# Kernel optimization log

Hardware: AMD Instinct MI355X
Metric: run time of the kernel (lower is better)

Reference implementation:

```python
import jax, jax.numpy as jnp
import numpy as np

N_HEADS = 8
NEG_INF = -1e9


def setup_inputs() -> dict:
    key = jax.random.key(0)
    ks = jax.random.split(key, 9)
    B, S, D = 4, 2048, 512
    scale = 1.0 / np.sqrt(D)
    x = jax.random.normal(ks[0], (B, S, D), dtype=jnp.float32)
    mask = jnp.tril(jnp.ones((S, S), dtype=bool))[None, None, :, :]  # causal [1,1,S,S]
    W_Q_w = jax.random.normal(ks[1], (D, D), dtype=jnp.float32) * scale
    W_Q_b = jax.random.normal(ks[2], (D,), dtype=jnp.float32) * 0.02
    W_K_w = jax.random.normal(ks[3], (D, D), dtype=jnp.float32) * scale
    W_K_b = jax.random.normal(ks[4], (D,), dtype=jnp.float32) * 0.02
    W_V_w = jax.random.normal(ks[5], (D, D), dtype=jnp.float32) * scale
    W_V_b = jax.random.normal(ks[6], (D,), dtype=jnp.float32) * 0.02
    W_O_w = jax.random.normal(ks[7], (D, D), dtype=jnp.float32) * scale
    W_O_b = jax.random.normal(ks[8], (D,), dtype=jnp.float32) * 0.02
    return {"x": x, "mask": mask,
            "W_Q_w": W_Q_w, "W_Q_b": W_Q_b, "W_K_w": W_K_w, "W_K_b": W_K_b,
            "W_V_w": W_V_w, "W_V_b": W_V_b, "W_O_w": W_O_w, "W_O_b": W_O_b}


def reference(x, mask, W_Q_w, W_Q_b, W_K_w, W_K_b, W_V_w, W_V_b, W_O_w, W_O_b):
    B, S, D = x.shape
    H = N_HEADS
    Dh = D // H
    # projections (torch Linear: x @ W.T + b), split heads -> [B,H,S,Dh]
    def split_heads(t):
        return t.reshape(B, S, H, Dh).transpose(0, 2, 1, 3)
    Q = split_heads(x @ W_Q_w.T + W_Q_b)
    K = split_heads(x @ W_K_w.T + W_K_b)
    V = split_heads(x @ W_V_w.T + W_V_b)
    # scaled dot-product attention with explicit [B,H,S,S] scores
    scores = jnp.einsum("bhqd,bhkd->bhqk", Q, K) / jnp.sqrt(jnp.float32(Dh))
    scores = jnp.where(mask, scores, jnp.float32(NEG_INF))
    att = jax.nn.softmax(scores, axis=-1)
    out = jnp.einsum("bhqk,bhkd->bhqd", att, V)
    out = out.transpose(0, 2, 1, 3).reshape(B, S, D)
    return out @ W_O_w.T + W_O_b
```

## Files before the change

kernel.cpp:

```cpp
#include <hip/hip_runtime.h>
#include <hip/hip_bf16.h>

#define BATCH 4
#define SEQ   2048
#define DIM   512
#define NH    8
#define DH    64
#define NTOK  (BATCH*SEQ)

typedef __bf16 bf16x8 __attribute__((ext_vector_type(8)));
typedef float  f32x4  __attribute__((ext_vector_type(4)));

#define MFMA16(a,b,c) __builtin_amdgcn_mfma_f32_16x16x32_bf16((a),(b),(c),0,0,0)

#if __has_builtin(__builtin_amdgcn_exp2f)
#define EXP2F(x) __builtin_amdgcn_exp2f(x)
#else
#define EXP2F(x) exp2f(x)
#endif

#define QSCALE 0.18033688011112042f
#define SMAX 16.0f

typedef __attribute__((address_space(1))) void GAS;
typedef __attribute__((address_space(3))) void LAS;
__device__ __forceinline__ void gl_lds16(const void* g, void* l) {
  __builtin_amdgcn_global_load_lds((GAS*)g, (LAS*)l, 16, 0, 0);
}

__global__ __launch_bounds__(256) void cvt_all(
    const float* __restrict__ x,
    const float* __restrict__ s0, const float* __restrict__ s1,
    const float* __restrict__ s2, const float* __restrict__ s3,
    __bf16* __restrict__ xb,
    __bf16* __restrict__ o0, __bf16* __restrict__ o1,
    __bf16* __restrict__ o2, __bf16* __restrict__ o3) {
  const int i = blockIdx.x * 256 + threadIdx.x;
  const float* src;
  __bf16* dst;
  int off;
  if (i < 524288) {
    src = x; dst = xb; off = i;
  } else {
    const int j = i - 524288;
    const int which = j >> 15; off = j & 32767;
    src = (which == 0) ? s0 : (which == 1) ? s1 : (which == 2) ? s2 : s3;
    dst = (which == 0) ? o0 : (which == 1) ? o1 : (which == 2) ? o2 : o3;
  }
  const float4* s = (const float4*)src;
  float4 a = s[2*off], b = s[2*off+1];
  bf16x8 o;
  o[0] = (__bf16)a.x; o[1] = (__bf16)a.y; o[2] = (__bf16)a.z; o[3] = (__bf16)a.w;
  o[4] = (__bf16)b.x; o[5] = (__bf16)b.y; o[6] = (__bf16)b.z; o[7] = (__bf16)b.w;
  *(bf16x8*)&dst[8*off] = o;
}

__global__ __launch_bounds__(256) void gemm_qkv(
    const __bf16* __restrict__ xb,
    const __bf16* __restrict__ wq, const __bf16* __restrict__ wk,
    const __bf16* __restrict__ wv,
    const float* __restrict__ bq, const float* __restrict__ bk,
    const float* __restrict__ bv,
    __bf16* __restrict__ Qb, __bf16* __restrict__ Kb, __bf16* __restrict__ Vt)
{
  const int z = blockIdx.z;
  const __bf16* W    = (z == 0) ? wq : (z == 1) ? wk : wv;
  const float*  bias = (z == 0) ? bq : (z == 1) ? bk : bv;

  __shared__ __align__(16) __bf16 smem[128*152];
  __bf16* As = smem;
  __bf16* Bs = smem + 128*64;

  const int tid  = threadIdx.x;
  const int m0   = blockIdx.x * 128, n0 = blockIdx.y * 128;
  const int w    = tid >> 6, lane = tid & 63, quad = lane >> 4, l16 = lane & 15;
  const int wm   = (w >> 1) * 64, wn = (w & 1) * 64;
  const int srow = w*32 + (lane >> 3);
  const int scc  = (lane & 7) * 8;

  f32x4 acc[4][4] = {};

  for (int k0 = 0; k0 < DIM; k0 += 64) {
#pragma unroll
    for (int i = 0; i < 4; ++i) {
      const int row = srow + i*8;
      gl_lds16(&xb[(size_t)(m0+row)*DIM + k0 + scc], &As[(w*4+i)*512]);
      gl_lds16(&W [(size_t)(n0+row)*DIM + k0 + scc], &Bs[(w*4+i)*512]);
    }
    __syncthreads();
#pragma unroll
    for (int kk = 0; kk < 2; ++kk) {
      const int ko = kk*32 + quad*8;
      bf16x8 af[4], bfr[4];
#pragma unroll
      for (int f = 0; f < 4; ++f) {
        af[f]  = *(const bf16x8*)&As[(wm + f*16 + l16)*64 + ko];
        bfr[f] = *(const bf16x8*)&Bs[(wn + f*16 + l16)*64 + ko];
      }
#pragma unroll
      for (int fm = 0; fm < 4; ++fm)
#pragma unroll
        for (int fn = 0; fn < 4; ++fn)
          acc[fm][fn] = MFMA16(af[fm], bfr[fn], acc[fm][fn]);
    }
    __syncthreads();
  }

  __bf16* Cs = smem;
#pragma unroll
  for (int fm = 0; fm < 4; ++fm) {
#pragma unroll
    for (int fn = 0; fn < 4; ++fn) {
      const int cl  = wn + fn*16 + l16;
      const float bc = bias[n0 + cl];
#pragma unroll
      for (int r = 0; r < 4; ++r) {
        const int rl = wm + fm*16 + quad*4 + r;
        float v = acc[fm][fn][r] + bc;
        if (z == 0) v *= QSCALE;
        Cs[rl*152 + cl] = (__bf16)v;
      }
    }
  }
  __syncthreads();

  if (z < 2) {
    const int r  = tid >> 1, hh = tid & 1;
    const int grow = m0 + r, b = grow >> 11, s = grow & 2047;
    const int h  = (n0 >> 6) + hh;
    __bf16* O = (z == 0) ? Qb : Kb;
    __bf16* dst = O + ((size_t)(b*NH + h)*SEQ + s)*DH;
    const __bf16* srcr = &Cs[r*152 + hh*64];
#pragma unroll
    for (int j = 0; j < 8; ++j)
      *(bf16x8*)&dst[j*8] = *(const bf16x8*)&srcr[j*8];
  } else {
    const int c  = tid >> 1, hh = tid & 1;
    const int col = n0 + c, h = col >> 6, dh = col & 63;
    const int b  = m0 >> 11, sbase = (m0 & 2047) + hh*64;
    __bf16* dst = Vt + ((size_t)(b*NH + h)*DH + dh)*SEQ + sbase;
#pragma unroll
    for (int j8 = 0; j8 < 8; ++j8) {
      bf16x8 o;
#pragma unroll
      for (int e = 0; e < 8; ++e)
        o[e] = Cs[(hh*64 + j8*8 + e)*152 + c];
      *(bf16x8*)&dst[j8*8] = o;
    }
  }
}

__global__ __launch_bounds__(256) void gemm_out(
    const __bf16* __restrict__ attnb, const __bf16* __restrict__ wo,
    const float* __restrict__ bo, float* __restrict__ out)
{
  __shared__ __align__(16) __bf16 As[64*64];
  __shared__ __align__(16) __bf16 Bs[128*64];

  const int tid = threadIdx.x;
  const int m0  = blockIdx.x * 64, n0 = blockIdx.y * 128;
  const int w   = tid >> 6, lane = tid & 63, quad = lane >> 4, l16 = lane & 15;
  const int wm  = (w >> 1) * 32, wn = (w & 1) * 64;
  const int srow = w*8 + (lane >> 3);
  const int scc  = (lane & 7) * 8;

  f32x4 acc[2][4] = {};

  for (int k0 = 0; k0 < DIM; k0 += 64) {
#pragma unroll
    for (int i = 0; i < 2; ++i)
      gl_lds16(&attnb[(size_t)(m0 + srow + i*32)*DIM + k0 + scc],
               &As[(i*4 + w)*512]);
#pragma unroll
    for (int i = 0; i < 4; ++i)
      gl_lds16(&wo[(size_t)(n0 + srow + i*32)*DIM + k0 + scc],
               &Bs[(i*4 + w)*512]);
    __syncthreads();
#pragma unroll
    for (int kk = 0; kk < 2; ++kk) {
      const int ko = kk*32 + quad*8;
      bf16x8 af[2], bfr[4];
#pragma unroll
      for (int f = 0; f < 2; ++f)
        af[f]  = *(const bf16x8*)&As[(wm + f*16 + l16)*64 + ko];
#pragma unroll
      for (int f = 0; f < 4; ++f)
        bfr[f] = *(const bf16x8*)&Bs[(wn + f*16 + l16)*64 + ko];
#pragma unroll
      for (int fm = 0; fm < 2; ++fm)
#pragma unroll
        for (int fn = 0; fn < 4; ++fn)
          acc[fm][fn] = MFMA16(af[fm], bfr[fn], acc[fm][fn]);
    }
    __syncthreads();
  }

#pragma unroll
  for (int fm = 0; fm < 2; ++fm) {
#pragma unroll
    for (int fn = 0; fn < 4; ++fn) {
      const int col  = n0 + wn + fn*16 + l16;
      const float bc = bo[col];
#pragma unroll
      for (int r = 0; r < 4; ++r) {
        const int row = m0 + wm + fm*16 + quad*4 + r;
        out[(size_t)row*DIM + col] = acc[fm][fn][r] + bc;
      }
    }
  }
}

__global__ __launch_bounds__(64) void flash_attn(
    const __bf16* __restrict__ Qb, const __bf16* __restrict__ Kb,
    const __bf16* __restrict__ Vt, __bf16* __restrict__ attnb)
{
  const int idx = blockIdx.x;
  const int bh  = idx & 31;
  const int t   = 63 - (idx >> 5);
  const int b   = bh >> 3, h = bh & 7;
  const int lane = threadIdx.x & 63, quad = lane >> 4, l16 = lane & 15;
  const int q0  = t * 32;

  const __bf16* Qp = Qb + (size_t)bh * SEQ * DH;
  const __bf16* Kp = Kb + (size_t)bh * SEQ * DH;
  const __bf16* Vp = Vt + (size_t)bh * DH * SEQ;

  __shared__ __align__(16) __bf16 Pw[32*88];

  bf16x8 qf[2][2];
#pragma unroll
  for (int mf = 0; mf < 2; ++mf)
#pragma unroll
    for (int kk = 0; kk < 2; ++kk)
      qf[mf][kk] = *(const bf16x8*)&Qp[(size_t)(q0 + mf*16 + l16)*DH + kk*32 + quad*8];

  f32x4 of[2][4] = {};
  float l_[2][4];
#pragma unroll
  for (int mf = 0; mf < 2; ++mf)
#pragma unroll
    for (int r = 0; r < 4; ++r) l_[mf][r] = 0.f;

  const int ktiles = (q0 >> 6) + 1;

  bf16x8 kfA[4][2], kfB[4][2];
#pragma unroll
  for (int fn = 0; fn < 4; ++fn)
#pragma unroll
    for (int kk = 0; kk < 2; ++kk)
      kfA[fn][kk] = *(const bf16x8*)&Kp[(size_t)(fn*16 + l16)*DH + kk*32 + quad*8];

#define TILE_STEP(KC, KN, KT)                                                  \
  {                                                                            \
    const int k0 = (KT) * 64;                                                  \
                   \
    bf16x8 vf[4][2];                                                           \
    _Pragma("unroll")                                                          \
    for (int nd = 0; nd < 4; ++nd)                                             \
      _Pragma("unroll")                                                        \
      for (int kq = 0; kq < 2; ++kq)                                           \
        vf[nd][kq] = *(const bf16x8*)&Vp[(size_t)(nd*16 + l16)*SEQ + k0 +      \
                                         kq*32 + quad*8];                      \
                               \
    {                                                                          \
      const int kn0 = ((KT) + 1 < ktiles) ? k0 + 64 : 0;                       \
      _Pragma("unroll")                                                        \
      for (int fn = 0; fn < 4; ++fn)                                           \
        _Pragma("unroll")                                                      \
        for (int kk = 0; kk < 2; ++kk)                                         \
          KN[fn][kk] = *(const bf16x8*)&Kp[(size_t)(kn0 + fn*16 + l16)*DH +    \
                                           kk*32 + quad*8];                    \
    }                                                                          \
                                   \
    f32x4 sf[2][4] = {};                                                       \
    __builtin_amdgcn_s_setprio(1);                                             \
    _Pragma("unroll")                                                          \
    for (int mf = 0; mf < 2; ++mf)                                             \
      _Pragma("unroll")                                                        \
      for (int fn = 0; fn < 4; ++fn) {                                         \
        sf[mf][fn] = MFMA16(qf[mf][0], KC[fn][0], sf[mf][fn]);                 \
        sf[mf][fn] = MFMA16(qf[mf][1], KC[fn][1], sf[mf][fn]);                 \
      }                                                                        \
    __builtin_amdgcn_s_setprio(0);                                             \
                               \
    if (k0 + 63 > q0) {                                                        \
      _Pragma("unroll")                                                        \
      for (int mf = 0; mf < 2; ++mf)                                           \
        _Pragma("unroll")                                                      \
        for (int fn = 0; fn < 4; ++fn) {                                       \
          const int col = k0 + fn*16 + l16;                                    \
          _Pragma("unroll")                                                    \
          for (int r = 0; r < 4; ++r) {                                        \
            const int row = q0 + mf*16 + quad*4 + r;                           \
            if (col > row) sf[mf][fn][r] = -1e30f;                             \
          }                                                                    \
        }                                                                      \
    }                                                                          \
                         \
    _Pragma("unroll")                                                          \
    for (int mf = 0; mf < 2; ++mf)                                             \
      _Pragma("unroll")                                                        \
      for (int fn = 0; fn < 4; ++fn)                                           \
        _Pragma("unroll")                                                      \
        for (int r = 0; r < 4; ++r)                                            \
          sf[mf][fn][r] = EXP2F(sf[mf][fn][r] - SMAX);                         \
    _Pragma("unroll")                                                          \
    for (int mf = 0; mf < 2; ++mf)                                             \
      _Pragma("unroll")                                                        \
      for (int r = 0; r < 4; ++r)                                              \
        l_[mf][r] += (sf[mf][0][r] + sf[mf][1][r]) +                           \
                     (sf[mf][2][r] + sf[mf][3][r]);                            \
                                           \
    _Pragma("unroll")                                                          \
    for (int mf = 0; mf < 2; ++mf)                                             \
      _Pragma("unroll")                                                        \
      for (int fn = 0; fn < 4; ++fn)                                           \
        _Pragma("unroll")                                                      \
        for (int r = 0; r < 4; ++r)                                            \
          Pw[(mf*16 + quad*4 + r)*88 + fn*16 + l16] = (__bf16)sf[mf][fn][r];   \
    bf16x8 pa[2][2];                                                           \
    _Pragma("unroll")                                                          \
    for (int mf = 0; mf < 2; ++mf)                                             \
      _Pragma("unroll")                                                        \
      for (int kq = 0; kq < 2; ++kq)                                           \
        pa[mf][kq] = *(const bf16x8*)&Pw[(mf*16 + l16)*88 + kq*32 + quad*8];   \
                                                      \
    __builtin_amdgcn_s_setprio(1);                                             \
    _Pragma("unroll")                                                          \
    for (int mf = 0; mf < 2; ++mf)                                             \
      _Pragma("unroll")                                                        \
      for (int nd = 0; nd < 4; ++nd) {                                         \
        of[mf][nd] = MFMA16(pa[mf][0], vf[nd][0], of[mf][nd]);                 \
        of[mf][nd] = MFMA16(pa[mf][1], vf[nd][1], of[mf][nd]);                 \
      }                                                                        \
    __builtin_amdgcn_s_setprio(0);                                             \
  }

  for (int kt = 0; kt < ktiles; kt += 2) {
    TILE_STEP(kfA, kfB, kt);
    if (kt + 1 < ktiles) TILE_STEP(kfB, kfA, kt + 1);
  }
#undef TILE_STEP

#pragma unroll
  for (int d = 1; d < 16; d <<= 1)
#pragma unroll
    for (int mf = 0; mf < 2; ++mf)
#pragma unroll
      for (int r = 0; r < 4; ++r)
        l_[mf][r] += __shfl_xor(l_[mf][r], d);
#pragma unroll
  for (int mf = 0; mf < 2; ++mf)
#pragma unroll
    for (int r = 0; r < 4; ++r)
      l_[mf][r] = 1.0f / l_[mf][r];
#pragma unroll
  for (int mf = 0; mf < 2; ++mf)
#pragma unroll
    for (int nd = 0; nd < 4; ++nd) {
      const int dh = nd*16 + l16;
#pragma unroll
      for (int r = 0; r < 4; ++r) {
        const int q = q0 + mf*16 + quad*4 + r;
        attnb[((size_t)b*SEQ + q)*DIM + h*DH + dh] = (__bf16)(of[mf][nd][r] * l_[mf][r]);
      }
    }
}

extern "C" void kernel_launch(void* const* d_in, const int* in_sizes, int n_in,
                              void* d_out, int out_size, void* d_ws, size_t ws_size,
                              hipStream_t stream) {
  const float* x  = (const float*)d_in[0];
  const float* Wq = (const float*)d_in[2];
  const float* bq = (const float*)d_in[3];
  const float* Wk = (const float*)d_in[4];
  const float* bk = (const float*)d_in[5];
  const float* Wv = (const float*)d_in[6];
  const float* bv = (const float*)d_in[7];
  const float* Wo = (const float*)d_in[8];
  const float* bo = (const float*)d_in[9];
  float* out = (float*)d_out;

  __bf16* xb    = (__bf16*)d_ws;
  __bf16* wq    = xb + (size_t)NTOK*DIM;
  __bf16* wk    = wq + DIM*DIM;
  __bf16* wv    = wk + DIM*DIM;
  __bf16* wo    = wv + DIM*DIM;
  __bf16* Qb    = wo + DIM*DIM;
  __bf16* Kb    = Qb + (size_t)NTOK*DIM;
  __bf16* Vt    = Kb + (size_t)NTOK*DIM;
  __bf16* attnb = Vt + (size_t)NTOK*DIM;

  cvt_all<<<2560, 256, 0, stream>>>(x, Wq, Wk, Wv, Wo, xb, wq, wk, wv, wo);

  gemm_qkv<<<dim3(NTOK/128, DIM/128, 3), 256, 0, stream>>>(
      xb, wq, wk, wv, bq, bk, bv, Qb, Kb, Vt);

  flash_attn<<<2048, 64, 0, stream>>>(Qb, Kb, Vt, attnb);

  gemm_out<<<dim3(NTOK/64, DIM/128), 256, 0, stream>>>(attnb, wo, bo, out);
}
```

Before: 200.2 us.

## Widen flash attention KV tile to 128 keys and reorder loads

The attention loop now processes 128 keys per iteration instead of 64 in unrolled pairs. It keeps 8 K fragments in registers and prefetches the next K tile after the QK MFMAs. The V loads are split into two halves, with the second half issued between the two softmax row groups. The P staging buffer grows to a 136-element stride, and the PV MFMAs are interleaved across both row fragments. The aim is to cut loop overhead and give loads more time to land, at the cost of higher register pressure and wasted masked work on the diagonal tile.

```diff
diff --git a/kernel.cpp b/kernel.cpp
--- a/kernel.cpp
+++ b/kernel.cpp
@@ -225,7 +225,7 @@
   const __bf16* Kp = Kb + (size_t)bh * SEQ * DH;
   const __bf16* Vp = Vt + (size_t)bh * DH * SEQ;
 
-  __shared__ __align__(16) __bf16 Pw[32*88];
+  __shared__ __align__(16) __bf16 Pw[32*136];
 
   bf16x8 qf[2][2];
 #pragma unroll
@@ -241,106 +241,99 @@
 #pragma unroll
     for (int r = 0; r < 4; ++r) l_[mf][r] = 0.f;
 
-  const int ktiles = (q0 >> 6) + 1;
-
-  bf16x8 kfA[4][2], kfB[4][2];
-#pragma unroll
-  for (int fn = 0; fn < 4; ++fn)
+  const int nsteps = (q0 + 32 + 127) >> 7;
+
+  bf16x8 kf[8][2];
+#pragma unroll
+  for (int fn = 0; fn < 8; ++fn)
 #pragma unroll
     for (int kk = 0; kk < 2; ++kk)
-      kfA[fn][kk] = *(const bf16x8*)&Kp[(size_t)(fn*16 + l16)*DH + kk*32 + quad*8];
-
-#define TILE_STEP(KC, KN, KT)                                                  \
-  {                                                                            \
-    const int k0 = (KT) * 64;                                                  \
-                   \
-    bf16x8 vf[4][2];                                                           \
-    _Pragma("unroll")                                                          \
-    for (int nd = 0; nd < 4; ++nd)                                             \
-      _Pragma("unroll")                                                        \
-      for (int kq = 0; kq < 2; ++kq)                                           \
-        vf[nd][kq] = *(const bf16x8*)&Vp[(size_t)(nd*16 + l16)*SEQ + k0 +      \
-                                         kq*32 + quad*8];                      \
-                               \
-    {                                                                          \
-      const int kn0 = ((KT) + 1 < ktiles) ? k0 + 64 : 0;                       \
-      _Pragma("unroll")                                                        \
-      for (int fn = 0; fn < 4; ++fn)                                           \
-        _Pragma("unroll")                                                      \
-        for (int kk = 0; kk < 2; ++kk)                                         \
-          KN[fn][kk] = *(const bf16x8*)&Kp[(size_t)(kn0 + fn*16 + l16)*DH +    \
-                                           kk*32 + quad*8];                    \
-    }                                                                          \
-                                   \
-    f32x4 sf[2][4] = {};                                                       \
-    __builtin_amdgcn_s_setprio(1);                                             \
-    _Pragma("unroll")                                                          \
-    for (int mf = 0; mf < 2; ++mf)                                             \
-      _Pragma("unroll")                                                        \
-      for (int fn = 0; fn < 4; ++fn) {                                         \
-        sf[mf][fn] = MFMA16(qf[mf][0], KC[fn][0], sf[mf][fn]);                 \
-        sf[mf][fn] = MFMA16(qf[mf][1], KC[fn][1], sf[mf][fn]);                 \
-      }                                                                        \
-    __builtin_amdgcn_s_setprio(0);                                             \
-                               \
-    if (k0 + 63 > q0) {                                                        \
-      _Pragma("unroll")                                                        \
-      for (int mf = 0; mf < 2; ++mf)                                           \
-        _Pragma("unroll")                                                      \
-        for (int fn = 0; fn < 4; ++fn) {                                       \
-          const int col = k0 + fn*16 + l16;                                    \
-          _Pragma("unroll")                                                    \
-          for (int r = 0; r < 4; ++r) {                                        \
-            const int row = q0 + mf*16 + quad*4 + r;                           \
-            if (col > row) sf[mf][fn][r] = -1e30f;                             \
-          }                                                                    \
-        }                                                                      \
-    }                                                                          \
-                         \
-    _Pragma("unroll")                                                          \
-    for (int mf = 0; mf < 2; ++mf)                                             \
-      _Pragma("unroll")                                                        \
-      for (int fn = 0; fn < 4; ++fn)                                           \
-        _Pragma("unroll")                                                      \
-        for (int r = 0; r < 4; ++r)                                            \
-          sf[mf][fn][r] = EXP2F(sf[mf][fn][r] - SMAX);                         \
-    _Pragma("unroll")                                                          \
-    for (int mf = 0; mf < 2; ++mf)                                             \
-      _Pragma("unroll")                                                        \
-      for (int r = 0; r < 4; ++r)                                              \
-        l_[mf][r] += (sf[mf][0][r] + sf[mf][1][r]) +                           \
-                     (sf[mf][2][r] + sf[mf][3][r]);                            \
-                                           \
-    _Pragma("unroll")                                                          \
-    for (int mf = 0; mf < 2; ++mf)                                             \
-      _Pragma("unroll")                                                        \
-      for (int fn = 0; fn < 4; ++fn)                                           \
-        _Pragma("unroll")                                                      \
-        for (int r = 0; r < 4; ++r)                                            \
-          Pw[(mf*16 + quad*4 + r)*88 + fn*16 + l16] = (__bf16)sf[mf][fn][r];   \
-    bf16x8 pa[2][2];                                                           \
-    _Pragma("unroll")                                                          \
-    for (int mf = 0; mf < 2; ++mf)                                             \
-      _Pragma("unroll")                                                        \
-      for (int kq = 0; kq < 2; ++kq)                                           \
-        pa[mf][kq] = *(const bf16x8*)&Pw[(mf*16 + l16)*88 + kq*32 + quad*8];   \
-                                                      \
-    __builtin_amdgcn_s_setprio(1);                                             \
-    _Pragma("unroll")                                                          \
-    for (int mf = 0; mf < 2; ++mf)                                             \
-      _Pragma("unroll")                                                        \
-      for (int nd = 0; nd < 4; ++nd) {                                         \
-        of[mf][nd] = MFMA16(pa[mf][0], vf[nd][0], of[mf][nd]);                 \
-        of[mf][nd] = MFMA16(pa[mf][1], vf[nd][1], of[mf][nd]);                 \
-      }                                                                        \
-    __builtin_amdgcn_s_setprio(0);                                             \
-  }
-
-  for (int kt = 0; kt < ktiles; kt += 2) {
-    TILE_STEP(kfA, kfB, kt);
-    if (kt + 1 < ktiles) TILE_STEP(kfB, kfA, kt + 1);
-  }
-#undef TILE_STEP
+      kf[fn][kk] = *(const bf16x8*)&Kp[(size_t)(fn*16 + l16)*DH + kk*32 + quad*8];
+
+  for (int kt = 0; kt < nsteps; ++kt) {
+    const int k0 = kt * 128;
+
+    bf16x8 vf[4][4];
+#pragma unroll
+    for (int nd = 0; nd < 4; ++nd)
+#pragma unroll
+      for (int kq = 0; kq < 2; ++kq)
+        vf[nd][kq] = *(const bf16x8*)&Vp[(size_t)(nd*16 + l16)*SEQ + k0 +
+                                         kq*32 + quad*8];
+
+    f32x4 sf[2][8] = {};
+    __builtin_amdgcn_s_setprio(1);
+#pragma unroll
+    for (int mf = 0; mf < 2; ++mf)
+#pragma unroll
+      for (int fn = 0; fn < 8; ++fn) {
+        sf[mf][fn] = MFMA16(qf[mf][0], kf[fn][0], sf[mf][fn]);
+        sf[mf][fn] = MFMA16(qf[mf][1], kf[fn][1], sf[mf][fn]);
+      }
+    __builtin_amdgcn_s_setprio(0);
+
+    {
+      const int kn0 = (kt + 1 < nsteps) ? k0 + 128 : 0;
+#pragma unroll
+      for (int fn = 0; fn < 8; ++fn)
+#pragma unroll
+        for (int kk = 0; kk < 2; ++kk)
+          kf[fn][kk] = *(const bf16x8*)&Kp[(size_t)(kn0 + fn*16 + l16)*DH +
+                                           kk*32 + quad*8];
+    }
+
+    if (k0 + 127 > q0) {
+#pragma unroll
+      for (int mf = 0; mf < 2; ++mf)
+#pragma unroll
+        for (int fn = 0; fn < 8; ++fn) {
+          const int col = k0 + fn*16 + l16;
+#pragma unroll
+          for (int r = 0; r < 4; ++r) {
+            const int row = q0 + mf*16 + quad*4 + r;
+            if (col > row) sf[mf][fn][r] = -1e30f;
+          }
+        }
+    }
+
+#pragma unroll
+    for (int fn = 0; fn < 8; ++fn)
+#pragma unroll
+      for (int r = 0; r < 4; ++r) {
+        const float p = EXP2F(sf[0][fn][r] - SMAX);
+        l_[0][r] += p;
+        Pw[(quad*4 + r)*136 + fn*16 + l16] = (__bf16)p;
+      }
+
+#pragma unroll
+    for (int nd = 0; nd < 4; ++nd)
+#pragma unroll
+      for (int kq = 2; kq < 4; ++kq)
+        vf[nd][kq] = *(const bf16x8*)&Vp[(size_t)(nd*16 + l16)*SEQ + k0 +
+                                         kq*32 + quad*8];
+
+#pragma unroll
+    for (int fn = 0; fn < 8; ++fn)
+#pragma unroll
+      for (int r = 0; r < 4; ++r) {
+        const float p = EXP2F(sf[1][fn][r] - SMAX);
+        l_[1][r] += p;
+        Pw[(16 + quad*4 + r)*136 + fn*16 + l16] = (__bf16)p;
+      }
+
+    __builtin_amdgcn_s_setprio(1);
+#pragma unroll
+    for (int kq = 0; kq < 4; ++kq) {
+      const bf16x8 pa0 = *(const bf16x8*)&Pw[(l16)*136 + kq*32 + quad*8];
+      const bf16x8 pa1 = *(const bf16x8*)&Pw[(16 + l16)*136 + kq*32 + quad*8];
+#pragma unroll
+      for (int nd = 0; nd < 4; ++nd) {
+        of[0][nd] = MFMA16(pa0, vf[nd][kq], of[0][nd]);
+        of[1][nd] = MFMA16(pa1, vf[nd][kq], of[1][nd]);
+      }
+    }
+    __builtin_amdgcn_s_setprio(0);
+  }
 
 #pragma unroll
   for (int d = 1; d < 16; d <<= 1)
```

Result: slower. 204.6 us (+2.2%).
